# Performance work log

Measured on AMD Instinct MI355X. Metric: run time of the kernel, lower is better.

## Reference

```python
import jax, jax.numpy as jnp
import numpy as np
import math

MODEL_DIM = 512
NUM_HEADS = 8
FFN_DIM = 2048
LN_EPS = 1e-5


def setup_inputs() -> dict:
    key = jax.random.key(0)
    ks = jax.random.split(key, 16)
    B, S, D, F = 1, 4096, MODEL_DIM, FFN_DIM
    s = 1.0 / math.sqrt(D)
    inp = {
        "x": jax.random.normal(ks[0], (B, S, D), dtype=jnp.float32),
        # Linear weights stored [in, out] (transpose of torch's [out, in]); y = x @ W + b
        "wq": jax.random.normal(ks[1], (D, D), dtype=jnp.float32) * s,
        "bq": jnp.zeros((D,), dtype=jnp.float32),
        "wk": jax.random.normal(ks[2], (D, D), dtype=jnp.float32) * s,
        "bk": jnp.zeros((D,), dtype=jnp.float32),
        "wv": jax.random.normal(ks[3], (D, D), dtype=jnp.float32) * s,
        "bv": jnp.zeros((D,), dtype=jnp.float32),
        "wo": jax.random.normal(ks[4], (D, D), dtype=jnp.float32) * s,
        "bo": jnp.zeros((D,), dtype=jnp.float32),
        "w1": jax.random.normal(ks[5], (D, F), dtype=jnp.float32) * s,
        "b1": jnp.zeros((F,), dtype=jnp.float32),
        "w2": jax.random.normal(ks[6], (F, D), dtype=jnp.float32) * (1.0 / math.sqrt(F)),
        "b2": jnp.zeros((D,), dtype=jnp.float32),
        "gamma": jnp.ones((D,), dtype=jnp.float32),
        "beta": jnp.zeros((D,), dtype=jnp.float32),
    }
    return inp


def _layer_norm(x, gamma, beta):
    mu = jnp.mean(x, axis=-1, keepdims=True)
    var = jnp.mean(jnp.square(x - mu), axis=-1, keepdims=True)
    return (x - mu) * jax.lax.rsqrt(var + LN_EPS) * gamma + beta


def reference(x, wq, bq, wk, bk, wv, bv, wo, bo, w1, b1, w2, b2, gamma, beta):
    B, S, D = x.shape
    H = NUM_HEADS
    dph = D // H
    q = x @ wq + bq
    k = x @ wk + bk
    v = x @ wv + bv
    # Faithful to original: direct view [B,S,D] -> [B*H, S, dph] (no head transpose)
    q = q.reshape(B * H, S, dph)
    k = k.reshape(B * H, S, dph)
    v = v.reshape(B * H, S, dph)
    scores = jnp.einsum('bqd,bkd->bqk', q, k) / math.sqrt(dph)  # [B*H, S, S]
    attn = jax.nn.softmax(scores, axis=-1)
    context = jnp.einsum('bqk,bkd->bqd', attn, v).reshape(B, S, D)
    attn_out = context @ wo + bo + x  # residual (dropout is identity in eval)
    ffn = jax.nn.relu(attn_out @ w1 + b1) @ w2 + b2
    out = _layer_norm(ffn + attn_out, gamma, beta)
    return out, attn
```

## Files before the change

kernel.cpp:

```cpp
#include <hip/hip_runtime.h>
#include <hip/hip_bf16.h>
#include <cstdint>
#include <cstddef>

#define SEQ 4096
#define DM  512
#define NH  8
#define DPH 64
#define FF  2048

using short8 = __attribute__((ext_vector_type(8))) short;
using f32x4  = __attribute__((ext_vector_type(4))) float;

__device__ inline float b2f(unsigned short u) {
    union { unsigned int i; float f; } c; c.i = ((unsigned int)u) << 16; return c.f;
}
__device__ inline unsigned short f2b(float f) {
    union { float f; unsigned int u; } c; c.f = f;
    unsigned int u = c.u;
    return (unsigned short)((u + 0x7fffu + ((u >> 16) & 1u)) >> 16);
}

template<int AF32>
__global__ __launch_bounds__(256) void gemm_kernel(
    const void* __restrict__ Av, const unsigned short* __restrict__ BT,
    const float* __restrict__ bias, const unsigned short* __restrict__ res,
    unsigned short* __restrict__ Cb, float* __restrict__ Cf,
    int M, int N, int K, long sA, long sB, long sC, float scale, int relu)
{
    const long z = blockIdx.z;
    BT += z * sB;
    const long co = z * sC;

    const int lane = threadIdx.x & 63;
    const int wid  = threadIdx.x >> 6;
    const int quad = lane >> 4;
    const int col  = lane & 15;
    const int m0 = blockIdx.y * 64 + wid * 16;
    const int n0 = blockIdx.x * 64;

    f32x4 acc[4];
    const f32x4 zero4 = {0.f, 0.f, 0.f, 0.f};
#pragma unroll
    for (int t = 0; t < 4; ++t) acc[t] = zero4;

    const unsigned short* arow16 = nullptr;
    const float*          arow32 = nullptr;
    if (AF32) arow32 = (const float*)Av          + z * sA + (size_t)(m0 + col) * K + quad * 8;
    else      arow16 = (const unsigned short*)Av + z * sA + (size_t)(m0 + col) * K + quad * 8;
    const unsigned short* brow = BT + (size_t)(n0 + col) * K + quad * 8;

    for (int k0 = 0; k0 < K; k0 += 32) {
        short8 a;
        if (AF32) {
            const float4 f0 = *(const float4*)(arow32 + k0);
            const float4 f1 = *(const float4*)(arow32 + k0 + 4);
            a[0] = (short)f2b(f0.x); a[1] = (short)f2b(f0.y);
            a[2] = (short)f2b(f0.z); a[3] = (short)f2b(f0.w);
            a[4] = (short)f2b(f1.x); a[5] = (short)f2b(f1.y);
            a[6] = (short)f2b(f1.z); a[7] = (short)f2b(f1.w);
        } else {
            a = *(const short8*)(arow16 + k0);
        }
#pragma unroll
        for (int t = 0; t < 4; ++t) {
            short8 b = *(const short8*)(brow + (size_t)t * 16 * K + k0);
            acc[t] = __builtin_amdgcn_mfma_f32_16x16x32_bf16(a, b, acc[t], 0, 0, 0);
        }
    }

#pragma unroll
    for (int t = 0; t < 4; ++t) {
        const int n = n0 + t * 16 + col;
        const float bv = bias ? bias[n] : 0.f;
#pragma unroll
        for (int r = 0; r < 4; ++r) {
            const int row = m0 + quad * 4 + r;
            float v = acc[t][r] * scale + bv;
            const size_t idx = (size_t)row * N + n;
            if (res)  v += b2f(res[idx]);
            if (relu) v = fmaxf(v, 0.f);
            if (Cf) Cf[co + idx] = v;
            else    Cb[co + idx] = f2b(v);
        }
    }
}

__global__ __launch_bounds__(256) void transpose_cast_kernel(
    const float* __restrict__ src, unsigned short* __restrict__ dst, int R, int C)
{
    __shared__ float tile[32][33];
    const int c0 = blockIdx.x * 32, r0 = blockIdx.y * 32;
    const int tx = threadIdx.x & 31, ty = threadIdx.x >> 5;
#pragma unroll
    for (int i = 0; i < 4; ++i)
        tile[ty + i * 8][tx] = src[(size_t)(r0 + ty + i * 8) * C + c0 + tx];
    __syncthreads();
#pragma unroll
    for (int i = 0; i < 4; ++i)
        dst[(size_t)(c0 + ty + i * 8) * R + r0 + tx] = f2b(tile[tx][ty + i * 8]);
}

__global__ __launch_bounds__(256) void transpose_kernel(
    const unsigned short* __restrict__ src, unsigned short* __restrict__ dst,
    int R, int C)
{
    __shared__ unsigned short tile[32][33];
    const long off = (long)blockIdx.z * (long)R * (long)C;
    src += off; dst += off;
    const int c0 = blockIdx.x * 32, r0 = blockIdx.y * 32;
    const int tx = threadIdx.x & 31, ty = threadIdx.x >> 5;
#pragma unroll
    for (int i = 0; i < 4; ++i)
        tile[ty + i * 8][tx] = src[(size_t)(r0 + ty + i * 8) * C + c0 + tx];
    __syncthreads();
#pragma unroll
    for (int i = 0; i < 4; ++i)
        dst[(size_t)(c0 + ty + i * 8) * R + r0 + tx] = tile[tx][ty + i * 8];
}

__global__ __launch_bounds__(256) void cast_kernel(
    const float* __restrict__ src, unsigned short* __restrict__ dst, int n4)
{
    const int i = blockIdx.x * 256 + threadIdx.x;
    if (i >= n4) return;
    const float4 v = ((const float4*)src)[i];
    union { unsigned short s[4]; unsigned long long u; } p;
    p.s[0] = f2b(v.x); p.s[1] = f2b(v.y); p.s[2] = f2b(v.z); p.s[3] = f2b(v.w);
    ((unsigned long long*)dst)[i] = p.u;
}

__global__ __launch_bounds__(256) void fused_attn_kernel(
    const unsigned short* __restrict__ qb,
    const unsigned short* __restrict__ kb,
    const unsigned short* __restrict__ vT,
    float* __restrict__ att,
    unsigned short* __restrict__ ctx)
{
    __shared__ __align__(16) float Pl[4][16 * 36];
    __shared__ float smM[4][16];
    __shared__ float smS[4][16];
    __shared__ __align__(16) float cbuf[2][16 * 65];

    const int id   = blockIdx.x;
    const int h    = id & 7;
    const int strip = id >> 3;
    const int lane = threadIdx.x & 63;
    const int w    = threadIdx.x >> 6;
    const int rh   = w >> 1, ch = w & 1;
    const int quad = lane >> 4, col = lane & 15;
    const int m0   = strip * 32 + rh * 16;

    const unsigned short* Qh = qb + (size_t)h * SEQ * DPH;
    const unsigned short* Kh = kb + (size_t)h * SEQ * DPH;
    const unsigned short* Vh = vT + (size_t)h * SEQ * DPH;
    float* atth = att + (size_t)h * SEQ * SEQ;
    unsigned short* ctxh = ctx + (size_t)h * SEQ * DPH;

    const unsigned short* qrow = Qh + (size_t)(m0 + col) * DPH + quad * 8;
    const short8 aq0 = *(const short8*)(qrow);
    const short8 aq1 = *(const short8*)(qrow + 32);

    const unsigned short* kbase = Kh + (size_t)(ch * 2048 + col) * DPH + quad * 8;
    const float SC = 0.125f;
    const f32x4 zero4 = {0.f, 0.f, 0.f, 0.f};

    float m[4], s[4];
#pragma unroll
    for (int r = 0; r < 4; ++r) { m[r] = -1e30f; s[r] = 0.f; }

#pragma unroll 2
    for (int nt = 0; nt < 128; ++nt) {
        const unsigned short* kr = kbase + (size_t)nt * 16 * DPH;
        const short8 b0 = *(const short8*)(kr);
        const short8 b1 = *(const short8*)(kr + 32);
        f32x4 acc = zero4;
        acc = __builtin_amdgcn_mfma_f32_16x16x32_bf16(aq0, b0, acc, 0, 0, 0);
        acc = __builtin_amdgcn_mfma_f32_16x16x32_bf16(aq1, b1, acc, 0, 0, 0);
#pragma unroll
        for (int r = 0; r < 4; ++r) {
            const float v  = acc[r] * SC;
            const float nm = fmaxf(m[r], v);
            s[r] = s[r] * __expf(m[r] - nm) + __expf(v - nm);
            m[r] = nm;
        }
    }
#pragma unroll
    for (int off = 1; off < 16; off <<= 1) {
#pragma unroll
        for (int r = 0; r < 4; ++r) {
            const float mo = __shfl_xor(m[r], off);
            const float so = __shfl_xor(s[r], off);
            const float nm = fmaxf(m[r], mo);
            s[r] = s[r] * __expf(m[r] - nm) + so * __expf(mo - nm);
            m[r] = nm;
        }
    }
    if (col == 0) {
#pragma unroll
        for (int r = 0; r < 4; ++r) { smM[w][quad * 4 + r] = m[r]; smS[w][quad * 4 + r] = s[r]; }
    }
    __syncthreads();
    float inv[4];
#pragma unroll
    for (int r = 0; r < 4; ++r) {
        const float mo = smM[w ^ 1][quad * 4 + r];
        const float so = smS[w ^ 1][quad * 4 + r];
        const float nm = fmaxf(m[r], mo);
        s[r] = s[r] * __expf(m[r] - nm) + so * __expf(mo - nm);
        m[r] = nm;
        inv[r] = 1.f / s[r];
    }

    f32x4 cacc[4];
#pragma unroll
    for (int t = 0; t < 4; ++t) cacc[t] = zero4;

    float* Pw = Pl[w];
    for (int pr = 0; pr < 64; ++pr) {
#pragma unroll
        for (int sub = 0; sub < 2; ++sub) {
            const int ntl = pr * 2 + sub;
            const unsigned short* kr = kbase + (size_t)ntl * 16 * DPH;
            const short8 b0 = *(const short8*)(kr);
            const short8 b1 = *(const short8*)(kr + 32);
            f32x4 acc = zero4;
            acc = __builtin_amdgcn_mfma_f32_16x16x32_bf16(aq0, b0, acc, 0, 0, 0);
            acc = __builtin_amdgcn_mfma_f32_16x16x32_bf16(aq1, b1, acc, 0, 0, 0);
            const int cg = ch * 2048 + ntl * 16 + col;
            float* arow = atth + (size_t)(m0 + quad * 4) * SEQ + cg;
#pragma unroll
            for (int r = 0; r < 4; ++r) {
                const float p = __expf(acc[r] * SC - m[r]) * inv[r];
                arow[(size_t)r * SEQ] = p;
                Pw[(quad * 4 + r) * 36 + sub * 16 + col] = p;
            }
        }
        const float4 pa0 = *(const float4*)(Pw + col * 36 + quad * 8);
        const float4 pa1 = *(const float4*)(Pw + col * 36 + quad * 8 + 4);
        union { unsigned short us[8]; short8 v; } ap;
        ap.us[0] = f2b(pa0.x); ap.us[1] = f2b(pa0.y);
        ap.us[2] = f2b(pa0.z); ap.us[3] = f2b(pa0.w);
        ap.us[4] = f2b(pa1.x); ap.us[5] = f2b(pa1.y);
        ap.us[6] = f2b(pa1.z); ap.us[7] = f2b(pa1.w);

        const int kg = ch * 2048 + pr * 32;
        const unsigned short* vb0 = Vh + (size_t)col * SEQ + kg + quad * 8;
#pragma unroll
        for (int t = 0; t < 4; ++t) {
            const short8 bv = *(const short8*)(vb0 + (size_t)t * 16 * SEQ);
            cacc[t] = __builtin_amdgcn_mfma_f32_16x16x32_bf16(ap.v, bv, cacc[t], 0, 0, 0);
        }
    }

    if (ch == 1) {
#pragma unroll
        for (int t = 0; t < 4; ++t)
#pragma unroll
            for (int r = 0; r < 4; ++r)
                cbuf[rh][(quad * 4 + r) * 65 + t * 16 + col] = cacc[t][r];
    }
    __syncthreads();
    if (ch == 0) {
#pragma unroll
        for (int t = 0; t < 4; ++t) {
#pragma unroll
            for (int r = 0; r < 4; ++r) {
                const float v = cacc[t][r] + cbuf[rh][(quad * 4 + r) * 65 + t * 16 + col];
                ctxh[(size_t)(m0 + quad * 4 + r) * DPH + t * 16 + col] = f2b(v);
            }
        }
    }
}

__global__ __launch_bounds__(256) void ln_kernel(
    const float* __restrict__ pre,
    const float* __restrict__ gamma, const float* __restrict__ beta,
    float* __restrict__ out)
{
    __shared__ float redS[4], redQ[4];
    const float* p = pre + (size_t)blockIdx.x * 512;
    const int t = threadIdx.x;
    const int w = t >> 6, lane = t & 63;

    const float2 xv = *(const float2*)(p + t * 2);
    float s = xv.x + xv.y;
    float q = xv.x * xv.x + xv.y * xv.y;
#pragma unroll
    for (int off = 32; off; off >>= 1) {
        s += __shfl_xor(s, off);
        q += __shfl_xor(q, off);
    }
    if (lane == 0) { redS[w] = s; redQ[w] = q; }
    __syncthreads();
    s = redS[0] + redS[1] + redS[2] + redS[3];
    q = redQ[0] + redQ[1] + redQ[2] + redQ[3];

    const float mu  = s * (1.f / 512.f);
    const float var = q * (1.f / 512.f) - mu * mu;
    const float rs  = rsqrtf(var + 1e-5f);

    const size_t o = (size_t)blockIdx.x * 512 + t * 2;
    out[o]     = (xv.x - mu) * rs * gamma[t * 2]     + beta[t * 2];
    out[o + 1] = (xv.y - mu) * rs * gamma[t * 2 + 1] + beta[t * 2 + 1];
}

extern "C" void kernel_launch(void* const* d_in, const int* in_sizes, int n_in,
                              void* d_out, int out_size, void* d_ws, size_t ws_size,
                              hipStream_t stream)
{
    (void)in_sizes; (void)n_in; (void)out_size; (void)ws_size;

    const float* x     = (const float*)d_in[0];
    const float* wq    = (const float*)d_in[1];
    const float* bq    = (const float*)d_in[2];
    const float* wk    = (const float*)d_in[3];
    const float* bk    = (const float*)d_in[4];
    const float* wv    = (const float*)d_in[5];
    const float* bv    = (const float*)d_in[6];
    const float* wo    = (const float*)d_in[7];
    const float* bo    = (const float*)d_in[8];
    const float* w1    = (const float*)d_in[9];
    const float* b1    = (const float*)d_in[10];
    const float* w2    = (const float*)d_in[11];
    const float* b2    = (const float*)d_in[12];
    const float* gamma = (const float*)d_in[13];
    const float* beta  = (const float*)d_in[14];

    float* out = (float*)d_out;
    float* att = out + (size_t)SEQ * DM;

    char* wsp = (char*)d_ws;
    auto alloc = [&](size_t bytes) {
        char* p = wsp;
        wsp += (bytes + 255) & ~(size_t)255;
        return p;
    };
    unsigned short* wqT  = (unsigned short*)alloc((size_t)DM * DM * 2);
    unsigned short* wkT  = (unsigned short*)alloc((size_t)DM * DM * 2);
    unsigned short* wvT  = (unsigned short*)alloc((size_t)DM * DM * 2);
    unsigned short* woT  = (unsigned short*)alloc((size_t)DM * DM * 2);
    unsigned short* w1T  = (unsigned short*)alloc((size_t)DM * FF * 2);
    unsigned short* w2T  = (unsigned short*)alloc((size_t)FF * DM * 2);
    unsigned short* xb   = (unsigned short*)alloc((size_t)SEQ * DM * 2);
    unsigned short* qb   = (unsigned short*)alloc((size_t)SEQ * DM * 2);
    unsigned short* kb   = (unsigned short*)alloc((size_t)SEQ * DM * 2);
    unsigned short* vb   = (unsigned short*)alloc((size_t)SEQ * DM * 2);
    unsigned short* vT   = (unsigned short*)alloc((size_t)SEQ * DM * 2);
    unsigned short* ctx  = (unsigned short*)alloc((size_t)SEQ * DM * 2);
    unsigned short* aout = (unsigned short*)alloc((size_t)SEQ * DM * 2);
    unsigned short* ffn1 = (unsigned short*)alloc((size_t)SEQ * FF * 2);
    float*          pre  = (float*)alloc((size_t)SEQ * DM * 4);

    const dim3 blk(256);

    cast_kernel<<<dim3((SEQ * DM / 4 + 255) / 256), blk, 0, stream>>>(x, xb, SEQ * DM / 4);

    transpose_cast_kernel<<<dim3(16, 16), blk, 0, stream>>>(wq, wqT, DM, DM);
    transpose_cast_kernel<<<dim3(16, 16), blk, 0, stream>>>(wk, wkT, DM, DM);
    transpose_cast_kernel<<<dim3(16, 16), blk, 0, stream>>>(wv, wvT, DM, DM);
    transpose_cast_kernel<<<dim3(16, 16), blk, 0, stream>>>(wo, woT, DM, DM);
    transpose_cast_kernel<<<dim3(64, 16), blk, 0, stream>>>(w1, w1T, DM, FF);
    transpose_cast_kernel<<<dim3(16, 64), blk, 0, stream>>>(w2, w2T, FF, DM);

    gemm_kernel<0><<<dim3(8, 64, 1), blk, 0, stream>>>(xb, wqT, bq, nullptr, qb, nullptr,
                                                       SEQ, DM, DM, 0, 0, 0, 1.f, 0);
    gemm_kernel<0><<<dim3(8, 64, 1), blk, 0, stream>>>(xb, wkT, bk, nullptr, kb, nullptr,
                                                       SEQ, DM, DM, 0, 0, 0, 1.f, 0);
    gemm_kernel<0><<<dim3(8, 64, 1), blk, 0, stream>>>(xb, wvT, bv, nullptr, vb, nullptr,
                                                       SEQ, DM, DM, 0, 0, 0, 1.f, 0);

    transpose_kernel<<<dim3(2, 128, 8), blk, 0, stream>>>(vb, vT, SEQ, DPH);

    fused_attn_kernel<<<dim3(1024), blk, 0, stream>>>(qb, kb, vT, att, ctx);

    gemm_kernel<0><<<dim3(8, 64, 1), blk, 0, stream>>>(ctx, woT, bo, xb, aout, nullptr,
                                                       SEQ, DM, DM, 0, 0, 0, 1.f, 0);

    gemm_kernel<0><<<dim3(32, 64, 1), blk, 0, stream>>>(aout, w1T, b1, nullptr, ffn1, nullptr,
                                                        SEQ, FF, DM, 0, 0, 0, 1.f, 1);

    gemm_kernel<0><<<dim3(8, 64, 1), blk, 0, stream>>>(ffn1, w2T, b2, aout, nullptr, pre,
                                                       SEQ, DM, FF, 0, 0, 0, 1.f, 0);

    ln_kernel<<<dim3(SEQ), blk, 0, stream>>>(pre, gamma, beta, out);
}
```

Baseline: 1.151 ms.

## Split attention key range across four waves per 16-row strip, doubling grid size

```diff
diff --git a/kernel.cpp b/kernel.cpp
--- a/kernel.cpp
+++ b/kernel.cpp
@@ -130,7 +130,7 @@
     ((unsigned long long*)dst)[i] = p.u;
 }
 
-__global__ __launch_bounds__(256) void fused_attn_kernel(
+__global__ __launch_bounds__(256, 8) void fused_attn_kernel(
     const unsigned short* __restrict__ qb,
     const unsigned short* __restrict__ kb,
     const unsigned short* __restrict__ vT,
@@ -140,16 +140,15 @@
     __shared__ __align__(16) float Pl[4][16 * 36];
     __shared__ float smM[4][16];
     __shared__ float smS[4][16];
-    __shared__ __align__(16) float cbuf[2][16 * 65];
-
-    const int id   = blockIdx.x;
-    const int h    = id & 7;
+    __shared__ __align__(16) float cbuf[2][16 * 68];
+
+    const int id    = blockIdx.x;
+    const int h     = id & 7;
     const int strip = id >> 3;
-    const int lane = threadIdx.x & 63;
-    const int w    = threadIdx.x >> 6;
-    const int rh   = w >> 1, ch = w & 1;
-    const int quad = lane >> 4, col = lane & 15;
-    const int m0   = strip * 32 + rh * 16;
+    const int lane  = threadIdx.x & 63;
+    const int w     = threadIdx.x >> 6;
+    const int quad  = lane >> 4, col = lane & 15;
+    const int m0    = strip * 16;
 
     const unsigned short* Qh = qb + (size_t)h * SEQ * DPH;
     const unsigned short* Kh = kb + (size_t)h * SEQ * DPH;
@@ -161,7 +160,7 @@
     const short8 aq0 = *(const short8*)(qrow);
     const short8 aq1 = *(const short8*)(qrow + 32);
 
-    const unsigned short* kbase = Kh + (size_t)(ch * 2048 + col) * DPH + quad * 8;
+    const unsigned short* kbase = Kh + (size_t)(w * 1024 + col) * DPH + quad * 8;
     const float SC = 0.125f;
     const f32x4 zero4 = {0.f, 0.f, 0.f, 0.f};
 
@@ -170,7 +169,7 @@
     for (int r = 0; r < 4; ++r) { m[r] = -1e30f; s[r] = 0.f; }
 
 #pragma unroll 2
-    for (int nt = 0; nt < 128; ++nt) {
+    for (int nt = 0; nt < 64; ++nt) {
         const unsigned short* kr = kbase + (size_t)nt * 16 * DPH;
         const short8 b0 = *(const short8*)(kr);
         const short8 b1 = *(const short8*)(kr + 32);
@@ -181,7 +180,8 @@
         for (int r = 0; r < 4; ++r) {
             const float v  = acc[r] * SC;
             const float nm = fmaxf(m[r], v);
-            s[r] = s[r] * __expf(m[r] - nm) + __expf(v - nm);
+            const float e  = __expf(fminf(m[r], v) - nm);
+            s[r] = (v > m[r]) ? fmaf(s[r], e, 1.f) : (s[r] + e);
             m[r] = nm;
         }
     }
@@ -204,12 +204,18 @@
     float inv[4];
 #pragma unroll
     for (int r = 0; r < 4; ++r) {
-        const float mo = smM[w ^ 1][quad * 4 + r];
-        const float so = smS[w ^ 1][quad * 4 + r];
-        const float nm = fmaxf(m[r], mo);
-        s[r] = s[r] * __expf(m[r] - nm) + so * __expf(mo - nm);
-        m[r] = nm;
-        inv[r] = 1.f / s[r];
+        const int row = quad * 4 + r;
+        float M = smM[0][row], S = smS[0][row];
+#pragma unroll
+        for (int ww = 1; ww < 4; ++ww) {
+            const float mo = smM[ww][row];
+            const float so = smS[ww][row];
+            const float nm = fmaxf(M, mo);
+            S = S * __expf(M - nm) + so * __expf(mo - nm);
+            M = nm;
+        }
+        m[r] = M;
+        inv[r] = 1.f / S;
     }
 
     f32x4 cacc[4];
@@ -217,7 +223,8 @@
     for (int t = 0; t < 4; ++t) cacc[t] = zero4;
 
     float* Pw = Pl[w];
-    for (int pr = 0; pr < 64; ++pr) {
+    float* abase = atth + (size_t)(m0 + quad * 4) * SEQ + w * 1024 + col;
+    for (int pr = 0; pr < 32; ++pr) {
 #pragma unroll
         for (int sub = 0; sub < 2; ++sub) {
             const int ntl = pr * 2 + sub;
@@ -227,11 +234,10 @@
             f32x4 acc = zero4;
             acc = __builtin_amdgcn_mfma_f32_16x16x32_bf16(aq0, b0, acc, 0, 0, 0);
             acc = __builtin_amdgcn_mfma_f32_16x16x32_bf16(aq1, b1, acc, 0, 0, 0);
-            const int cg = ch * 2048 + ntl * 16 + col;
-            float* arow = atth + (size_t)(m0 + quad * 4) * SEQ + cg;
+            float* arow = abase + ntl * 16;
 #pragma unroll
             for (int r = 0; r < 4; ++r) {
-                const float p = __expf(acc[r] * SC - m[r]) * inv[r];
+                const float p = __expf(fmaf(acc[r], SC, -m[r])) * inv[r];
                 arow[(size_t)r * SEQ] = p;
                 Pw[(quad * 4 + r) * 36 + sub * 16 + col] = p;
             }
@@ -244,7 +250,7 @@
         ap.us[4] = f2b(pa1.x); ap.us[5] = f2b(pa1.y);
         ap.us[6] = f2b(pa1.z); ap.us[7] = f2b(pa1.w);
 
-        const int kg = ch * 2048 + pr * 32;
+        const int kg = w * 1024 + pr * 32;
         const unsigned short* vb0 = Vh + (size_t)col * SEQ + kg + quad * 8;
 #pragma unroll
         for (int t = 0; t < 4; ++t) {
@@ -253,20 +259,38 @@
         }
     }
 
-    if (ch == 1) {
+    if (w & 1) {
+        float* cb = cbuf[w >> 1];
 #pragma unroll
         for (int t = 0; t < 4; ++t)
 #pragma unroll
             for (int r = 0; r < 4; ++r)
-                cbuf[rh][(quad * 4 + r) * 65 + t * 16 + col] = cacc[t][r];
-    }
-    __syncthreads();
-    if (ch == 0) {
+                cb[(quad * 4 + r) * 68 + t * 16 + col] = cacc[t][r];
+    }
+    __syncthreads();
+    if (!(w & 1)) {
+        const float* cb = cbuf[w >> 1];
+#pragma unroll
+        for (int t = 0; t < 4; ++t)
+#pragma unroll
+            for (int r = 0; r < 4; ++r)
+                cacc[t][r] += cb[(quad * 4 + r) * 68 + t * 16 + col];
+    }
+    __syncthreads();
+    if (w == 2) {
+#pragma unroll
+        for (int t = 0; t < 4; ++t)
+#pragma unroll
+            for (int r = 0; r < 4; ++r)
+                cbuf[0][(quad * 4 + r) * 68 + t * 16 + col] = cacc[t][r];
+    }
+    __syncthreads();
+    if (w == 0) {
 #pragma unroll
         for (int t = 0; t < 4; ++t) {
 #pragma unroll
             for (int r = 0; r < 4; ++r) {
-                const float v = cacc[t][r] + cbuf[rh][(quad * 4 + r) * 65 + t * 16 + col];
+                const float v = cacc[t][r] + cbuf[0][(quad * 4 + r) * 68 + t * 16 + col];
                 ctxh[(size_t)(m0 + quad * 4 + r) * DPH + t * 16 + col] = f2b(v);
             }
         }
@@ -372,7 +396,7 @@
 
     transpose_kernel<<<dim3(2, 128, 8), blk, 0, stream>>>(vb, vT, SEQ, DPH);
 
-    fused_attn_kernel<<<dim3(1024), blk, 0, stream>>>(qb, kb, vT, att, ctx);
+    fused_attn_kernel<<<dim3(2048), blk, 0, stream>>>(qb, kb, vT, att, ctx);
 
     gemm_kernel<0><<<dim3(8, 64, 1), blk, 0, stream>>>(ctx, woT, bo, xb, aout, nullptr,
                                                        SEQ, DM, DM, 0, 0, 0, 1.f, 0);
```

New measurement: 1.165 ms. No clear change (+1.2%).
